# Performance work log

Measured on AMD Instinct MI355X. Metric: run time of the kernel, lower is better.

The kernel has to match this reference:

```python
import jax, jax.numpy as jnp
import numpy as np

N_NODES = 131072       # 64 graphs * 2048 nodes
N_EDGES = 2097152      # avg degree 16
N_GRAPHS = 64
NODES_PER_GRAPH = 2048
D_IN = 128
D_EMB = 64
D_HID = 128
N_ACT = 2048


def setup_inputs() -> dict:
    key = jax.random.key(0)
    ks = jax.random.split(key, 12)
    s = lambda d: 1.0 / np.sqrt(d)
    return {
        "x": jax.random.normal(ks[0], (N_NODES, D_IN), dtype=jnp.float32),
        "edge_index": jax.random.randint(ks[1], (2, N_EDGES), 0, N_NODES, dtype=jnp.int32),
        "W1l": jax.random.normal(ks[2], (D_EMB, D_IN), dtype=jnp.float32) * s(D_IN),
        "b1l": jnp.zeros((D_EMB,), dtype=jnp.float32),
        "W1r": jax.random.normal(ks[3], (D_EMB, D_IN), dtype=jnp.float32) * s(D_IN),
        "W2l": jax.random.normal(ks[4], (D_EMB, D_EMB), dtype=jnp.float32) * s(D_EMB),
        "b2l": jnp.zeros((D_EMB,), dtype=jnp.float32),
        "W2r": jax.random.normal(ks[5], (D_EMB, D_EMB), dtype=jnp.float32) * s(D_EMB),
        "fc1_W": jax.random.normal(ks[6], (D_HID, D_EMB), dtype=jnp.float32) * s(D_EMB),
        "fc1_b": jnp.zeros((D_HID,), dtype=jnp.float32),
        "fc2_W": jax.random.normal(ks[7], (N_ACT, D_HID), dtype=jnp.float32) * s(D_HID),
        "fc2_b": jnp.zeros((N_ACT,), dtype=jnp.float32),
    }


def _sage_conv(x, src, dst, Wl, bl, Wr):
    # PyG SAGEConv (mean aggr): out = lin_l(mean_{j in N(i)} x_j) + lin_r(x_i)
    msg = x[src]                                              # [E, D] gather
    agg = jax.ops.segment_sum(msg, dst, num_segments=N_NODES)  # [N, D]
    cnt = jax.ops.segment_sum(jnp.ones((src.shape[0],), x.dtype), dst,
                              num_segments=N_NODES)
    mean = agg / jnp.maximum(cnt, 1.0)[:, None]
    return mean @ Wl.T + bl + x @ Wr.T


def reference(x, edge_index, W1l, b1l, W1r, W2l, b2l, W2r,
              fc1_W, fc1_b, fc2_W, fc2_b):
    src, dst = edge_index[0], edge_index[1]
    h1 = _sage_conv(x, src, dst, W1l, b1l, W1r)    # [N, D_EMB]
    h2 = _sage_conv(h1, src, dst, W2l, b2l, W2r)   # [N, D_EMB]
    g = h2.reshape(N_GRAPHS, NODES_PER_GRAPH, D_EMB).mean(axis=1)  # [B, D_EMB]
    h = jax.nn.relu(g @ fc1_W.T + fc1_b)
    q_values = h @ fc2_W.T + fc2_b                 # [B, N_ACT]
    return q_values
```

## Files before the change

### kernel.cpp

```cpp
#include <hip/hip_runtime.h>
#include <hip/hip_bf16.h>

#define D_IN 128
#define D_EMB 64

typedef float f32x2 __attribute__((ext_vector_type(2)));
typedef float f32x4v __attribute__((ext_vector_type(4)));
typedef short bf16x8 __attribute__((ext_vector_type(8)));

static __device__ __forceinline__ unsigned short f2bf(float f) {
  __hip_bfloat16 h = __float2bfloat16(f);
  return *(unsigned short*)&h;
}

__global__ __launch_bounds__(256) void wprep_mfma_k(const float* __restrict__ W,
                                                    unsigned short* __restrict__ out,
                                                    int K) {
  int tid = blockIdx.x * 256 + threadIdx.x;
  int total = (K / 32) * 4 * 64;
  if (tid >= total) return;
  int lane = tid & 63;
  int ct = (tid >> 6) & 3;
  int s = tid >> 8;
  int row = ct * 16 + (lane & 15);
  int kk = s * 32 + (lane >> 4) * 8;
  unsigned short tmp[8];
#pragma unroll
  for (int j = 0; j < 8; j++) tmp[j] = f2bf(W[row * K + kk + j]);
  *(uint4*)&out[(size_t)tid * 8] = *(uint4*)tmp;
}


__global__ __launch_bounds__(256) void bhist1_k(const int* __restrict__ key,
                                                int* __restrict__ bh, int E) {
  __shared__ int h[256];
  const int t = threadIdx.x;
  h[t] = 0;
  __syncthreads();
  const int base = blockIdx.x * 2048;
#pragma unroll
  for (int j = 0; j < 8; j++) {
    int e = base + j * 256 + t;
    if (e < E) atomicAdd(&h[key[e] >> 9], 1);
  }
  __syncthreads();
  bh[t * 1024 + blockIdx.x] = h[t];
}

__global__ __launch_bounds__(256) void scanA_k(int* __restrict__ bh,
                                               int* __restrict__ bintot) {
  __shared__ int sa[256], sb[256];
  const int t = threadIdx.x;
  int* row = bh + (size_t)blockIdx.x * 1024;
  int v0 = row[t * 4], v1 = row[t * 4 + 1], v2 = row[t * 4 + 2], v3 = row[t * 4 + 3];
  int sum = v0 + v1 + v2 + v3;
  sa[t] = sum;
  __syncthreads();
  int* in = sa;
  int* out = sb;
  for (int st = 1; st < 256; st <<= 1) {
    out[t] = in[t] + (t >= st ? in[t - st] : 0);
    __syncthreads();
    int* tmp = in; in = out; out = tmp;
  }
  int excl = in[t] - sum;
  row[t * 4] = excl;
  row[t * 4 + 1] = excl + v0;
  row[t * 4 + 2] = excl + v0 + v1;
  row[t * 4 + 3] = excl + v0 + v1 + v2;
  if (t == 255) bintot[blockIdx.x] = in[255];
}

__global__ __launch_bounds__(256) void scanB_k(const int* __restrict__ bintot,
                                               int* __restrict__ base) {
  __shared__ int sa[256], sb[256];
  const int t = threadIdx.x;
  int v = bintot[t];
  sa[t] = v;
  __syncthreads();
  int* in = sa;
  int* out = sb;
  for (int st = 1; st < 256; st <<= 1) {
    out[t] = in[t] + (t >= st ? in[t - st] : 0);
    __syncthreads();
    int* tmp = in; in = out; out = tmp;
  }
  base[t] = in[t] - v;
  if (t == 255) base[256] = in[255];
}

__global__ __launch_bounds__(256) void sfill_k(const int* __restrict__ src,
                                               const int* __restrict__ dst,
                                               const int* __restrict__ sh,
                                               const int* __restrict__ ssub,
                                               int* __restrict__ srcS,
                                               int* __restrict__ dstS, int E) {
  __shared__ int hA[256], hB[256], runCur[256], gb[256];
  __shared__ int scache[2048];
  __shared__ int dcache[2048];
  __shared__ int sortS[2048];
  __shared__ int sortD[2048];
  __shared__ unsigned short subb[2048];
  const int t = threadIdx.x;
  const int base = blockIdx.x * 2048;
  const int n = min(2048, E - base);
  hA[t] = 0;
  __syncthreads();
#pragma unroll
  for (int j = 0; j < 8; j++) {
    int idx = j * 256 + t;
    int e = base + idx;
    if (idx < n) {
      int s = src[e];
      scache[idx] = s;
      dcache[idx] = dst[e];
      atomicAdd(&hA[s >> 9], 1);
    }
  }
  __syncthreads();
  int cnt = hA[t];
  int* in = hA;
  int* out = hB;
  for (int st = 1; st < 256; st <<= 1) {
    out[t] = in[t] + (t >= st ? in[t - st] : 0);
    __syncthreads();
    int* tmp = in; in = out; out = tmp;
  }
  int rs = in[t] - cnt;
  __syncthreads();
  hB[t] = rs;
  runCur[t] = rs;
  gb[t] = ssub[t] + sh[t * 1024 + blockIdx.x];
  __syncthreads();
#pragma unroll
  for (int j = 0; j < 8; j++) {
    int idx = j * 256 + t;
    if (idx < n) {
      int s = scache[idx];
      int b = s >> 9;
      int lpos = atomicAdd(&runCur[b], 1);
      sortS[lpos] = s;
      sortD[lpos] = dcache[idx];
      subb[lpos] = (unsigned short)b;
    }
  }
  __syncthreads();
  for (int idx = t; idx < n; idx += 256) {
    int b = subb[idx];
    int g = gb[b] + idx - hB[b];
    srcS[g] = sortS[idx];
    dstS[g] = sortD[idx];
  }
}

__global__ __launch_bounds__(256) void bfill1_k(const int* __restrict__ src,
                                                const int* __restrict__ dst,
                                                const int* __restrict__ bh,
                                                const int* __restrict__ sbase,
                                                unsigned int* __restrict__ bkt,
                                                int E) {
  __shared__ int hA[256], hB[256], runCur[256], gb[256];
  __shared__ int dcache[2048];
  __shared__ unsigned int sorted[2048];
  __shared__ unsigned short subb[2048];
  const int t = threadIdx.x;
  const int base = blockIdx.x * 2048;
  const int n = min(2048, E - base);
  hA[t] = 0;
  __syncthreads();
#pragma unroll
  for (int j = 0; j < 8; j++) {
    int idx = j * 256 + t;
    int e = base + idx;
    if (idx < n) {
      int d = dst[e];
      dcache[idx] = d;
      atomicAdd(&hA[d >> 9], 1);
    }
  }
  __syncthreads();
  int cnt = hA[t];
  int* in = hA;
  int* out = hB;
  for (int st = 1; st < 256; st <<= 1) {
    out[t] = in[t] + (t >= st ? in[t - st] : 0);
    __syncthreads();
    int* tmp = in; in = out; out = tmp;
  }
  int rs = in[t] - cnt;
  __syncthreads();
  hB[t] = rs;
  runCur[t] = rs;
  gb[t] = sbase[t] + bh[t * 1024 + blockIdx.x];
  __syncthreads();
#pragma unroll
  for (int j = 0; j < 8; j++) {
    int idx = j * 256 + t;
    int e = base + idx;
    if (idx < n) {
      int d = dcache[idx];
      int b = d >> 9;
      int lpos = atomicAdd(&runCur[b], 1);
      sorted[lpos] = ((unsigned)(d & 511) << 17) | (unsigned)src[e];
      subb[lpos] = (unsigned short)b;
    }
  }
  __syncthreads();
  for (int idx = t; idx < n; idx += 256) {
    int b = subb[idx];
    bkt[gb[b] + idx - hB[b]] = sorted[idx];
  }
}

__global__ __launch_bounds__(256) void deg4_k(const unsigned int* __restrict__ bkt,
                                              const int* __restrict__ sbase,
                                              int* __restrict__ deg) {
  __shared__ int h[512];
  const int t = threadIdx.x;
  h[t] = 0;
  h[t + 256] = 0;
  __syncthreads();
  const int i = blockIdx.x;
  const int lo = sbase[i], hi = sbase[i + 1];
  for (int e = lo + t; e < hi; e += 256) atomicAdd(&h[bkt[e] >> 17], 1);
  __syncthreads();
  deg[i * 512 + t] = h[t];
  deg[i * 512 + t + 256] = h[t + 256];
}

__global__ __launch_bounds__(256) void blocksum_k(const int* __restrict__ deg,
                                                  int* __restrict__ bsum) {
  __shared__ int sm[256];
  int t = threadIdx.x;
  sm[t] = deg[blockIdx.x * 256 + t];
  __syncthreads();
  for (int s = 128; s > 0; s >>= 1) {
    if (t < s) sm[t] += sm[t + s];
    __syncthreads();
  }
  if (t == 0) bsum[blockIdx.x] = sm[0];
}

__global__ __launch_bounds__(256) void scanbsum_k(int* __restrict__ bsum) {
  __shared__ int a[512], b[512];
  int t = threadIdx.x;
  a[t] = bsum[t];
  a[t + 256] = bsum[t + 256];
  __syncthreads();
  int* in = a;
  int* out = b;
  for (int st = 1; st < 512; st <<= 1) {
    for (int i = t; i < 512; i += 256) out[i] = in[i] + (i >= st ? in[i - st] : 0);
    __syncthreads();
    int* tmp = in; in = out; out = tmp;
  }
  for (int i = t; i < 512; i += 256) bsum[i] = (i == 0) ? 0 : in[i - 1];
}

__global__ __launch_bounds__(256) void rowptr_k(const int* __restrict__ deg,
                                                const int* __restrict__ bsumEx,
                                                int* __restrict__ rowPtr,
                                                float* __restrict__ invdeg) {
  __shared__ int a[256], b[256];
  int t = threadIdx.x;
  int i = blockIdx.x * 256 + t;
  int d = deg[i];
  a[t] = d;
  __syncthreads();
  int* in = a;
  int* out = b;
  for (int st = 1; st < 256; st <<= 1) {
    out[t] = in[t] + (t >= st ? in[t - st] : 0);
    __syncthreads();
    int* tmp = in; in = out; out = tmp;
  }
  int incl = in[t] + bsumEx[blockIdx.x];
  rowPtr[i + 1] = incl;
  invdeg[i] = 1.0f / fmaxf((float)d, 1.0f);
  if (i == 0) rowPtr[0] = 0;
}

#define CSR_CAP 12032
__global__ __launch_bounds__(256) void scat4_k(const unsigned int* __restrict__ bkt,
                                               const int* __restrict__ sbase,
                                               const int* __restrict__ rowPtr,
                                               int* __restrict__ csr) {
  __shared__ int cur[512];
  __shared__ int cbuf[CSR_CAP];
  const int t = threadIdx.x;
  const int i = blockIdx.x;
  const int node0 = i * 512;
  const int base0 = rowPtr[node0];
  cur[t] = rowPtr[node0 + t] - base0;
  cur[t + 256] = rowPtr[node0 + t + 256] - base0;
  __syncthreads();
  const int lo = sbase[i], hi = sbase[i + 1];
  for (int e = lo + t; e < hi; e += 256) {
    unsigned v = bkt[e];
    int pos = atomicAdd(&cur[v >> 17], 1);
    int sval = (int)(v & 0x1FFFFu);
    if (pos < CSR_CAP) cbuf[pos] = sval;
    else csr[base0 + pos] = sval;
  }
  __syncthreads();
  const int cnt = rowPtr[node0 + 512] - base0;
  const int lim = cnt < CSR_CAP ? cnt : CSR_CAP;
  for (int idx = t; idx < lim; idx += 256) csr[base0 + idx] = cbuf[idx];
}

__global__ __launch_bounds__(256) void gemm1_k(const float4* __restrict__ x4,
                                               const unsigned short* __restrict__ wb1,
                                               const unsigned short* __restrict__ wb2,
                                               const float* __restrict__ bias2,
                                               unsigned char* __restrict__ out1,
                                               float* __restrict__ out2) {
  constexpr int K = 128, K4 = K / 4;
  const int t = threadIdx.x;
  const int lane = t & 63;
  const int wv = t >> 6;
  const int col = lane & 15;
  const int quad = lane >> 4;
  const int nb = blockIdx.x * 64;
  const int arow = nb + wv * 16 + col;
  f32x4v acc1[4], acc2[4];
#pragma unroll
  for (int ct = 0; ct < 4; ct++) {
    acc1[ct] = (f32x4v){0.f, 0.f, 0.f, 0.f};
    float bj = bias2[ct * 16 + col];
    acc2[ct] = (f32x4v){bj, bj, bj, bj};
  }
#pragma unroll
  for (int s = 0; s < K / 32; s++) {
    float4 f0 = x4[(size_t)arow * K4 + s * 8 + quad * 2];
    float4 f1 = x4[(size_t)arow * K4 + s * 8 + quad * 2 + 1];
    unsigned short h[8];
    h[0] = f2bf(f0.x); h[1] = f2bf(f0.y); h[2] = f2bf(f0.z); h[3] = f2bf(f0.w);
    h[4] = f2bf(f1.x); h[5] = f2bf(f1.y); h[6] = f2bf(f1.z); h[7] = f2bf(f1.w);
    bf16x8 a = *(const bf16x8*)h;
#pragma unroll
    for (int ct = 0; ct < 4; ct++) {
      bf16x8 b1 = *(const bf16x8*)&wb1[(size_t)((s * 4 + ct) * 64 + lane) * 8];
      acc1[ct] = __builtin_amdgcn_mfma_f32_16x16x32_bf16(a, b1, acc1[ct], 0, 0, 0);
      bf16x8 b2 = *(const bf16x8*)&wb2[(size_t)((s * 4 + ct) * 64 + lane) * 8];
      acc2[ct] = __builtin_amdgcn_mfma_f32_16x16x32_bf16(a, b2, acc2[ct], 0, 0, 0);
    }
  }
#pragma unroll
  for (int ct = 0; ct < 4; ct++) {
#pragma unroll
    for (int reg = 0; reg < 4; reg++) {
      int node = nb + wv * 16 + quad * 4 + reg;
      unsigned pk = (unsigned)__builtin_amdgcn_cvt_pk_fp8_f32(acc1[ct][reg],
                                                              acc1[ct][reg], 0, false);
      out1[(size_t)node * 64 + ct * 16 + col] = (unsigned char)(pk & 0xff);
      out2[(size_t)node * 64 + ct * 16 + col] = acc2[ct][reg];
    }
  }
}

#define LROW 72
__global__ __launch_bounds__(256) void gatherf_k(const uint4* __restrict__ yb,
                                                 const int* __restrict__ csr,
                                                 const int* __restrict__ rowPtr,
                                                 const float* __restrict__ invdeg,
                                                 const float4* __restrict__ xr,
                                                 const unsigned short* __restrict__ wb2,
                                                 unsigned char* __restrict__ y2,
                                                 float* __restrict__ pm) {
  __shared__ float sg[4][4][16];
  __shared__ unsigned short sh1[64 * LROW];
  const int t = threadIdx.x;
  const int lane = t & 63;
  const int wv = t >> 6;
  const int q = lane & 3;
  const int nl = lane >> 2;
  const int nb = blockIdx.x * 64;
  const int n = nb + wv * 16 + nl;
  const int rp0 = rowPtr[n], rp1 = rowPtr[n + 1];
  float acc[16];
#pragma unroll
  for (int k = 0; k < 16; k++) acc[k] = 0.f;
  for (int e = rp0; e < rp1; e++) {
    int s = csr[e];
    uint4 v = yb[(size_t)s * 4 + q];
    f32x2 p;
    p = __builtin_amdgcn_cvt_pk_f32_fp8(v.x, false); acc[0] += p.x;  acc[1] += p.y;
    p = __builtin_amdgcn_cvt_pk_f32_fp8(v.x, true);  acc[2] += p.x;  acc[3] += p.y;
    p = __builtin_amdgcn_cvt_pk_f32_fp8(v.y, false); acc[4] += p.x;  acc[5] += p.y;
    p = __builtin_amdgcn_cvt_pk_f32_fp8(v.y, true);  acc[6] += p.x;  acc[7] += p.y;
    p = __builtin_amdgcn_cvt_pk_f32_fp8(v.z, false); acc[8] += p.x;  acc[9] += p.y;
    p = __builtin_amdgcn_cvt_pk_f32_fp8(v.z, true);  acc[10] += p.x; acc[11] += p.y;
    p = __builtin_amdgcn_cvt_pk_f32_fp8(v.w, false); acc[12] += p.x; acc[13] += p.y;
    p = __builtin_amdgcn_cvt_pk_f32_fp8(v.w, true);  acc[14] += p.x; acc[15] += p.y;
  }
  const float sc = invdeg[n];
  float gacc[16];
  {
    const int nloc = wv * 16 + nl;
    unsigned short hh[16];
#pragma unroll
    for (int u = 0; u < 4; u++) {
      float4 o = xr[(size_t)n * 16 + q * 4 + u];
      float v0 = acc[4 * u + 0] * sc + o.x;
      float v1 = acc[4 * u + 1] * sc + o.y;
      float v2 = acc[4 * u + 2] * sc + o.z;
      float v3 = acc[4 * u + 3] * sc + o.w;
      gacc[4 * u + 0] = v0; gacc[4 * u + 1] = v1;
      gacc[4 * u + 2] = v2; gacc[4 * u + 3] = v3;
      hh[4 * u + 0] = f2bf(v0); hh[4 * u + 1] = f2bf(v1);
      hh[4 * u + 2] = f2bf(v2); hh[4 * u + 3] = f2bf(v3);
    }
    *(uint4*)&sh1[nloc * LROW + q * 16] = *(uint4*)&hh[0];
    *(uint4*)&sh1[nloc * LROW + q * 16 + 8] = *(uint4*)&hh[8];
  }
#pragma unroll
  for (int m = 4; m <= 32; m <<= 1)
#pragma unroll
    for (int k = 0; k < 16; k++) gacc[k] += __shfl_xor(gacc[k], m, 64);
  if (nl == 0) {
#pragma unroll
    for (int k = 0; k < 16; k++) sg[wv][q][k] = gacc[k];
  }
  __syncthreads();
  if (t < 64) {
    int qq = t >> 4, k = t & 15;
    float tot = sg[0][qq][k] + sg[1][qq][k] + sg[2][qq][k] + sg[3][qq][k];
    pm[((size_t)(blockIdx.x >> 5) * 32 + (blockIdx.x & 31)) * 64 + t] = tot;
  }
  {
    const int col = lane & 15;
    const int quad = lane >> 4;
    f32x4v a2[4];
#pragma unroll
    for (int ct = 0; ct < 4; ct++) a2[ct] = (f32x4v){0.f, 0.f, 0.f, 0.f};
#pragma unroll
    for (int s = 0; s < 2; s++) {
      bf16x8 a = *(const bf16x8*)&sh1[(wv * 16 + col) * LROW + s * 32 + quad * 8];
#pragma unroll
      for (int ct = 0; ct < 4; ct++) {
        bf16x8 b = *(const bf16x8*)&wb2[(size_t)((s * 4 + ct) * 64 + lane) * 8];
        a2[ct] = __builtin_amdgcn_mfma_f32_16x16x32_bf16(a, b, a2[ct], 0, 0, 0);
      }
    }
#pragma unroll
    for (int ct = 0; ct < 4; ct++) {
#pragma unroll
      for (int reg = 0; reg < 4; reg++) {
        int node = nb + wv * 16 + quad * 4 + reg;
        unsigned pk = (unsigned)__builtin_amdgcn_cvt_pk_fp8_f32(a2[ct][reg],
                                                                a2[ct][reg], 0, false);
        y2[(size_t)node * 64 + ct * 16 + col] = (unsigned char)(pk & 0xff);
      }
    }
  }
}

__global__ __launch_bounds__(256) void gatherp_k(const uint4* __restrict__ yb,
                                                 const int* __restrict__ csr,
                                                 const int* __restrict__ rowPtr,
                                                 const float* __restrict__ invdeg,
                                                 float* __restrict__ pm) {
  __shared__ float sg[4][4][16];
  const int t = threadIdx.x;
  const int lane = t & 63;
  const int wv = t >> 6;
  const int q = lane & 3;
  const int nl = lane >> 2;
  const int nb = blockIdx.x * 64;
  const int n = nb + wv * 16 + nl;
  const int rp0 = rowPtr[n], rp1 = rowPtr[n + 1];
  float acc[16];
#pragma unroll
  for (int k = 0; k < 16; k++) acc[k] = 0.f;
  for (int e = rp0; e < rp1; e++) {
    int s = csr[e];
    uint4 v = yb[(size_t)s * 4 + q];
    f32x2 p;
    p = __builtin_amdgcn_cvt_pk_f32_fp8(v.x, false); acc[0] += p.x;  acc[1] += p.y;
    p = __builtin_amdgcn_cvt_pk_f32_fp8(v.x, true);  acc[2] += p.x;  acc[3] += p.y;
    p = __builtin_amdgcn_cvt_pk_f32_fp8(v.y, false); acc[4] += p.x;  acc[5] += p.y;
    p = __builtin_amdgcn_cvt_pk_f32_fp8(v.y, true);  acc[6] += p.x;  acc[7] += p.y;
    p = __builtin_amdgcn_cvt_pk_f32_fp8(v.z, false); acc[8] += p.x;  acc[9] += p.y;
    p = __builtin_amdgcn_cvt_pk_f32_fp8(v.z, true);  acc[10] += p.x; acc[11] += p.y;
    p = __builtin_amdgcn_cvt_pk_f32_fp8(v.w, false); acc[12] += p.x; acc[13] += p.y;
    p = __builtin_amdgcn_cvt_pk_f32_fp8(v.w, true);  acc[14] += p.x; acc[15] += p.y;
  }
  const float sc = invdeg[n];
  float gacc[16];
#pragma unroll
  for (int k = 0; k < 16; k++) gacc[k] = acc[k] * sc;
#pragma unroll
  for (int m = 4; m <= 32; m <<= 1)
#pragma unroll
    for (int k = 0; k < 16; k++) gacc[k] += __shfl_xor(gacc[k], m, 64);
  if (nl == 0) {
#pragma unroll
    for (int k = 0; k < 16; k++) sg[wv][q][k] = gacc[k];
  }
  __syncthreads();
  if (t < 64) {
    int qq = t >> 4, k = t & 15;
    float tot = sg[0][qq][k] + sg[1][qq][k] + sg[2][qq][k] + sg[3][qq][k];
    pm[((size_t)(blockIdx.x >> 5) * 32 + (blockIdx.x & 31)) * 64 + t] = tot;
  }
}

__global__ __launch_bounds__(256) void reduce_part_k(const float* __restrict__ pm,
                                                     float* __restrict__ gm) {
  int idx = blockIdx.x * 256 + threadIdx.x;
  int b = idx >> 6, j = idx & 63;
  float acc = 0.0f;
  for (int blk = 0; blk < 32; blk++) acc += pm[((size_t)b * 32 + blk) * 64 + j];
  gm[idx] = acc * (1.0f / 2048.0f);
}

__global__ __launch_bounds__(256) void combine_k(const float* __restrict__ gmean2,
                                                 const float* __restrict__ gmean1,
                                                 const float* __restrict__ b2l,
                                                 const float* __restrict__ W2r,
                                                 float* __restrict__ g) {
  int idx = blockIdx.x * 256 + threadIdx.x;
  int b = idx >> 6, j = idx & 63;
  const float4* m4 = (const float4*)(gmean1 + b * 64);
  const float4* w4 = (const float4*)(W2r + j * 64);
  float acc = gmean2[idx] + b2l[j];
#pragma unroll
  for (int k4 = 0; k4 < 16; k4++) {
    float4 mv = m4[k4], wv = w4[k4];
    acc += mv.x * wv.x + mv.y * wv.y + mv.z * wv.z + mv.w * wv.w;
  }
  g[idx] = acc;
}

__global__ __launch_bounds__(256) void mlp1_k(const float* __restrict__ g,
                                              const float* __restrict__ fc1_W,
                                              const float* __restrict__ fc1_b,
                                              float* __restrict__ h) {
  int idx = blockIdx.x * 256 + threadIdx.x;
  int b = idx >> 7, k = idx & 127;
  const float4* g4 = (const float4*)(g + b * 64);
  const float4* w4 = (const float4*)(fc1_W + k * 64);
  float acc = fc1_b[k];
#pragma unroll
  for (int j4 = 0; j4 < 16; j4++) {
    float4 gv = g4[j4], wv = w4[j4];
    acc += gv.x * wv.x + gv.y * wv.y + gv.z * wv.z + gv.w * wv.w;
  }
  h[idx] = fmaxf(acc, 0.0f);
}

__global__ __launch_bounds__(256) void mlp2_k(const float* __restrict__ h,
                                              const float* __restrict__ fc2_W,
                                              const float* __restrict__ fc2_b,
                                              float* __restrict__ out) {
  __shared__ float4 sh[32];
  int b = blockIdx.x >> 3;
  int a = (blockIdx.x & 7) * 256 + threadIdx.x;
  if (threadIdx.x < 32) sh[threadIdx.x] = ((const float4*)(h + b * 128))[threadIdx.x];
  __syncthreads();
  const float4* w4 = (const float4*)(fc2_W + (size_t)a * 128);
  float acc = fc2_b[a];
#pragma unroll
  for (int k4 = 0; k4 < 32; k4++) {
    float4 hv = sh[k4], wv = w4[k4];
    acc += hv.x * wv.x + hv.y * wv.y + hv.z * wv.z + hv.w * wv.w;
  }
  out[b * 2048 + a] = acc;
}

extern "C" void kernel_launch(void* const* d_in, const int* in_sizes, int n_in,
                              void* d_out, int out_size, void* d_ws, size_t ws_size,
                              hipStream_t stream) {
  const float* x     = (const float*)d_in[0];
  const int*   ei    = (const int*)d_in[1];
  const float* W1l   = (const float*)d_in[2];
  const float* b1l   = (const float*)d_in[3];
  const float* W1r   = (const float*)d_in[4];
  const float* W2l   = (const float*)d_in[5];
  const float* b2l   = (const float*)d_in[6];
  const float* W2r   = (const float*)d_in[7];
  const float* fc1_W = (const float*)d_in[8];
  const float* fc1_b = (const float*)d_in[9];
  const float* fc2_W = (const float*)d_in[10];
  const float* fc2_b = (const float*)d_in[11];
  float* out = (float*)d_out;

  const int N = in_sizes[0] / D_IN;
  const int E = in_sizes[1] / 2;
  const int* src = ei;
  const int* dst = ei + E;

  char* ws = (char*)d_ws;
  int*   deg    = (int*)ws;     ws += (size_t)N * 4;
  int*   rowPtr = (int*)ws;     ws += (size_t)(N + 256) * 4;
  int*   bsum   = (int*)ws;     ws += 512 * 4;
  float* invdeg = (float*)ws;   ws += (size_t)N * 4;
  float* gmean1 = (float*)ws;   ws += 4096 * 4;
  float* gmean2 = (float*)ws;   ws += 4096 * 4;
  float* g      = (float*)ws;   ws += 4096 * 4;
  float* hbuf   = (float*)ws;   ws += 8192 * 4;
  unsigned short* wb1l = (unsigned short*)ws;  ws += 8192 * 2;
  unsigned short* wb1r = (unsigned short*)ws;  ws += 8192 * 2;
  unsigned short* wb2l = (unsigned short*)ws;  ws += 4096 * 2;
  int*   sh     = (int*)ws;     ws += (size_t)256 * 1024 * 4;
  int*   bh     = (int*)ws;     ws += (size_t)256 * 1024 * 4;
  int*   tot    = (int*)ws;     ws += 256 * 4;
  int*   ssub   = (int*)ws;     ws += 260 * 4;
  int*   sbase  = (int*)ws;     ws += 260 * 4;
  float* p1     = (float*)ws;   ws += (size_t)64 * 32 * 64 * 4;
  float* p2     = (float*)ws;   ws += (size_t)64 * 32 * 64 * 4;
  unsigned int* bkt = (unsigned int*)ws;  ws += (size_t)E * 4;
  int*   csr    = (int*)ws;     ws += (size_t)E * 4;
  unsigned char* bufA = (unsigned char*)ws;  ws += (size_t)64 * N;
  unsigned char* bufD = (unsigned char*)ws;  ws += (size_t)64 * N;
  float* bufB   = (float*)ws;   ws += (size_t)64 * N * 4;
  size_t used = (size_t)(ws - (char*)d_ws);

  int* srcS = (int*)bufD;
  int* dstS = (int*)bufA;

  hipMemsetAsync(d_ws, 0, used, stream);

  wprep_mfma_k<<<4, 256, 0, stream>>>(W1l, wb1l, 128);
  wprep_mfma_k<<<4, 256, 0, stream>>>(W1r, wb1r, 128);
  wprep_mfma_k<<<2, 256, 0, stream>>>(W2l, wb2l, 64);

  const int nch = (E + 2047) >> 11;
  bhist1_k<<<nch, 256, 0, stream>>>(src, sh, E);
  scanA_k<<<256, 256, 0, stream>>>(sh, tot);
  scanB_k<<<1, 256, 0, stream>>>(tot, ssub);
  sfill_k<<<nch, 256, 0, stream>>>(src, dst, sh, ssub, srcS, dstS, E);
  bhist1_k<<<nch, 256, 0, stream>>>(dstS, bh, E);
  scanA_k<<<256, 256, 0, stream>>>(bh, tot);
  scanB_k<<<1, 256, 0, stream>>>(tot, sbase);
  bfill1_k<<<nch, 256, 0, stream>>>(srcS, dstS, bh, sbase, bkt, E);
  deg4_k<<<256, 256, 0, stream>>>(bkt, sbase, deg);
  blocksum_k<<<N / 256, 256, 0, stream>>>(deg, bsum);
  scanbsum_k<<<1, 256, 0, stream>>>(bsum);
  rowptr_k<<<N / 256, 256, 0, stream>>>(deg, bsum, rowPtr, invdeg);
  scat4_k<<<256, 256, 0, stream>>>(bkt, sbase, rowPtr, csr);

  gemm1_k<<<N / 64, 256, 0, stream>>>((const float4*)x, wb1l, wb1r, b1l, bufA, bufB);
  gatherf_k<<<N / 64, 256, 0, stream>>>((const uint4*)bufA, csr, rowPtr, invdeg,
                                        (const float4*)bufB, wb2l, bufD, p1);
  reduce_part_k<<<16, 256, 0, stream>>>(p1, gmean1);

  gatherp_k<<<N / 64, 256, 0, stream>>>((const uint4*)bufD, csr, rowPtr, invdeg, p2);
  reduce_part_k<<<16, 256, 0, stream>>>(p2, gmean2);

  combine_k<<<16, 256, 0, stream>>>(gmean2, gmean1, b2l, W2r, g);
  mlp1_k<<<32, 256, 0, stream>>>(g, fc1_W, fc1_b, hbuf);
  mlp2_k<<<512, 256, 0, stream>>>(hbuf, fc2_W, fc2_b, out);
}
```

Baseline: 352.6 us.

## Degree-sort nodes within 64-node blocks, store root term in bf16, merge reductions

Adds a kernel that ranks nodes by in-degree inside each 64-node group and gives the gather kernels this permutation. Lanes in a wavefront then process nodes of similar degree, which reduces divergence in the per-node edge loop. The root-term buffer from gemm1 is stored as bf16 instead of fp32 to halve its traffic, and the two partial-mean reductions are merged into one launch. The costs are an extra launch, an indirect node index and slightly lower precision in the root term.

```diff
diff --git a/kernel.cpp b/kernel.cpp
--- a/kernel.cpp
+++ b/kernel.cpp
@@ -11,6 +11,9 @@
 static __device__ __forceinline__ unsigned short f2bf(float f) {
   __hip_bfloat16 h = __float2bfloat16(f);
   return *(unsigned short*)&h;
+}
+static __device__ __forceinline__ float bf2f(unsigned short u) {
+  return __uint_as_float((unsigned)u << 16);
 }
 
 __global__ __launch_bounds__(256) void wprep_mfma_k(const float* __restrict__ W,
@@ -308,12 +311,30 @@
   for (int idx = t; idx < lim; idx += 256) csr[base0 + idx] = cbuf[idx];
 }
 
+__global__ __launch_bounds__(256) void nperm_k(const int* __restrict__ deg,
+                                               int* __restrict__ perm) {
+  __shared__ int dg[256];
+  const int t = threadIdx.x;
+  const int n0 = blockIdx.x * 256;
+  int myd = deg[n0 + t];
+  dg[t] = myd;
+  __syncthreads();
+  const int g0 = t & ~63;
+  int rank = 0;
+#pragma unroll
+  for (int j = 0; j < 64; j++) {
+    int dj = dg[g0 + j];
+    rank += (dj < myd) || (dj == myd && (g0 + j) < t);
+  }
+  perm[n0 + g0 + rank] = n0 + t;
+}
+
 __global__ __launch_bounds__(256) void gemm1_k(const float4* __restrict__ x4,
                                                const unsigned short* __restrict__ wb1,
                                                const unsigned short* __restrict__ wb2,
                                                const float* __restrict__ bias2,
                                                unsigned char* __restrict__ out1,
-                                               float* __restrict__ out2) {
+                                               unsigned short* __restrict__ out2) {
   constexpr int K = 128, K4 = K / 4;
   const int t = threadIdx.x;
   const int lane = t & 63;
@@ -353,7 +374,7 @@
       unsigned pk = (unsigned)__builtin_amdgcn_cvt_pk_fp8_f32(acc1[ct][reg],
                                                               acc1[ct][reg], 0, false);
       out1[(size_t)node * 64 + ct * 16 + col] = (unsigned char)(pk & 0xff);
-      out2[(size_t)node * 64 + ct * 16 + col] = acc2[ct][reg];
+      out2[(size_t)node * 64 + ct * 16 + col] = f2bf(acc2[ct][reg]);
     }
   }
 }
@@ -363,19 +384,22 @@
                                                  const int* __restrict__ csr,
                                                  const int* __restrict__ rowPtr,
                                                  const float* __restrict__ invdeg,
-                                                 const float4* __restrict__ xr,
+                                                 const unsigned short* __restrict__ xr,
+                                                 const int* __restrict__ perm,
                                                  const unsigned short* __restrict__ wb2,
                                                  unsigned char* __restrict__ y2,
                                                  float* __restrict__ pm) {
   __shared__ float sg[4][4][16];
   __shared__ unsigned short sh1[64 * LROW];
-  const int t = threadIdx.x;
+  __shared__ int sp[64];
+  const int t = threadIdx.x;
+  if (t < 64) sp[t] = perm[blockIdx.x * 64 + t];
+  __syncthreads();
   const int lane = t & 63;
   const int wv = t >> 6;
   const int q = lane & 3;
   const int nl = lane >> 2;
-  const int nb = blockIdx.x * 64;
-  const int n = nb + wv * 16 + nl;
+  const int n = sp[wv * 16 + nl];
   const int rp0 = rowPtr[n], rp1 = rowPtr[n + 1];
   float acc[16];
 #pragma unroll
@@ -400,11 +424,11 @@
     unsigned short hh[16];
 #pragma unroll
     for (int u = 0; u < 4; u++) {
-      float4 o = xr[(size_t)n * 16 + q * 4 + u];
-      float v0 = acc[4 * u + 0] * sc + o.x;
-      float v1 = acc[4 * u + 1] * sc + o.y;
-      float v2 = acc[4 * u + 2] * sc + o.z;
-      float v3 = acc[4 * u + 3] * sc + o.w;
+      ushort4 ob = *(const ushort4*)&xr[(size_t)n * 64 + q * 16 + u * 4];
+      float v0 = acc[4 * u + 0] * sc + bf2f(ob.x);
+      float v1 = acc[4 * u + 1] * sc + bf2f(ob.y);
+      float v2 = acc[4 * u + 2] * sc + bf2f(ob.z);
+      float v3 = acc[4 * u + 3] * sc + bf2f(ob.w);
       gacc[4 * u + 0] = v0; gacc[4 * u + 1] = v1;
       gacc[4 * u + 2] = v2; gacc[4 * u + 3] = v3;
       hh[4 * u + 0] = f2bf(v0); hh[4 * u + 1] = f2bf(v1);
@@ -446,7 +470,7 @@
     for (int ct = 0; ct < 4; ct++) {
 #pragma unroll
       for (int reg = 0; reg < 4; reg++) {
-        int node = nb + wv * 16 + quad * 4 + reg;
+        int node = sp[wv * 16 + quad * 4 + reg];
         unsigned pk = (unsigned)__builtin_amdgcn_cvt_pk_fp8_f32(a2[ct][reg],
                                                                 a2[ct][reg], 0, false);
         y2[(size_t)node * 64 + ct * 16 + col] = (unsigned char)(pk & 0xff);
@@ -459,15 +483,18 @@
                                                  const int* __restrict__ csr,
                                                  const int* __restrict__ rowPtr,
                                                  const float* __restrict__ invdeg,
+                                                 const int* __restrict__ perm,
                                                  float* __restrict__ pm) {
   __shared__ float sg[4][4][16];
-  const int t = threadIdx.x;
+  __shared__ int sp[64];
+  const int t = threadIdx.x;
+  if (t < 64) sp[t] = perm[blockIdx.x * 64 + t];
+  __syncthreads();
   const int lane = t & 63;
   const int wv = t >> 6;
   const int q = lane & 3;
   const int nl = lane >> 2;
-  const int nb = blockIdx.x * 64;
-  const int n = nb + wv * 16 + nl;
+  const int n = sp[wv * 16 + nl];
   const int rp0 = rowPtr[n], rp1 = rowPtr[n + 1];
   float acc[16];
 #pragma unroll
@@ -505,9 +532,14 @@
   }
 }
 
-__global__ __launch_bounds__(256) void reduce_part_k(const float* __restrict__ pm,
-                                                     float* __restrict__ gm) {
-  int idx = blockIdx.x * 256 + threadIdx.x;
+__global__ __launch_bounds__(256) void reduce_both_k(const float* __restrict__ p1,
+                                                     const float* __restrict__ p2,
+                                                     float* __restrict__ gm1,
+                                                     float* __restrict__ gm2) {
+  int half = blockIdx.x >> 4;
+  int idx = (blockIdx.x & 15) * 256 + threadIdx.x;
+  const float* pm = half ? p2 : p1;
+  float* gm = half ? gm2 : gm1;
   int b = idx >> 6, j = idx & 63;
   float acc = 0.0f;
   for (int blk = 0; blk < 32; blk++) acc += pm[((size_t)b * 32 + blk) * 64 + j];
@@ -595,6 +627,7 @@
   int*   rowPtr = (int*)ws;     ws += (size_t)(N + 256) * 4;
   int*   bsum   = (int*)ws;     ws += 512 * 4;
   float* invdeg = (float*)ws;   ws += (size_t)N * 4;
+  int*   perm   = (int*)ws;     ws += (size_t)N * 4;
   float* gmean1 = (float*)ws;   ws += 4096 * 4;
   float* gmean2 = (float*)ws;   ws += 4096 * 4;
   float* g      = (float*)ws;   ws += 4096 * 4;
@@ -613,7 +646,7 @@
   int*   csr    = (int*)ws;     ws += (size_t)E * 4;
   unsigned char* bufA = (unsigned char*)ws;  ws += (size_t)64 * N;
   unsigned char* bufD = (unsigned char*)ws;  ws += (size_t)64 * N;
-  float* bufB   = (float*)ws;   ws += (size_t)64 * N * 4;
+  unsigned short* bufB = (unsigned short*)ws;  ws += (size_t)64 * N * 2;
   size_t used = (size_t)(ws - (char*)d_ws);
 
   int* srcS = (int*)bufD;
@@ -639,14 +672,14 @@
   scanbsum_k<<<1, 256, 0, stream>>>(bsum);
   rowptr_k<<<N / 256, 256, 0, stream>>>(deg, bsum, rowPtr, invdeg);
   scat4_k<<<256, 256, 0, stream>>>(bkt, sbase, rowPtr, csr);
+  nperm_k<<<N / 256, 256, 0, stream>>>(deg, perm);
 
   gemm1_k<<<N / 64, 256, 0, stream>>>((const float4*)x, wb1l, wb1r, b1l, bufA, bufB);
   gatherf_k<<<N / 64, 256, 0, stream>>>((const uint4*)bufA, csr, rowPtr, invdeg,
-                                        (const float4*)bufB, wb2l, bufD, p1);
-  reduce_part_k<<<16, 256, 0, stream>>>(p1, gmean1);
-
-  gatherp_k<<<N / 64, 256, 0, stream>>>((const uint4*)bufD, csr, rowPtr, invdeg, p2);
-  reduce_part_k<<<16, 256, 0, stream>>>(p2, gmean2);
+                                        bufB, perm, wb2l, bufD, p1);
+  gatherp_k<<<N / 64, 256, 0, stream>>>((const uint4*)bufD, csr, rowPtr, invdeg,
+                                        perm, p2);
+  reduce_both_k<<<32, 256, 0, stream>>>(p1, p2, gmean1, gmean2);
 
   combine_k<<<16, 256, 0, stream>>>(gmean2, gmean1, b2l, W2r, g);
   mlp1_k<<<32, 256, 0, stream>>>(g, fc1_W, fc1_b, hbuf);
```

Measured after the change: 346.1 us. About the same (-1.8%).
